# Kernel tuning notes

Hardware: AMD Instinct MI355X
Metric: run time of the kernel (lower is better)

## Reference

```python
import jax, jax.numpy as jnp
import numpy as np

EMBED_DIM = 512
NUM_HEADS = 8
NUM_RULES = 16
HEAD_DIM = EMBED_DIM // NUM_HEADS


def setup_inputs() -> dict:
    key = jax.random.key(0)
    ks = jax.random.split(key, 10)
    B, S, E, H, R, D = 4, 2048, EMBED_DIM, NUM_HEADS, NUM_RULES, HEAD_DIM
    lim_q = 1.0 / np.sqrt(E)
    lim_v = 1.0 / np.sqrt(E)
    return {
        "query": jax.random.normal(ks[0], (B, S, E), jnp.float32),
        "key": jax.random.normal(ks[1], (B, S, E), jnp.float32),
        "value": jax.random.normal(ks[2], (B, S, E), jnp.float32),
        "Wq": jax.random.uniform(ks[3], (E, E), jnp.float32, -lim_q, lim_q),
        "bq": jax.random.uniform(ks[4], (E,), jnp.float32, -lim_q, lim_q),
        "Wv": jax.random.uniform(ks[5], (E * R, E), jnp.float32, -lim_v, lim_v),
        "bv": jax.random.uniform(ks[6], (E * R,), jnp.float32, -lim_v, lim_v),
        "Wo": jax.random.uniform(ks[7], (E, E), jnp.float32, -lim_q, lim_q),
        "bo": jax.random.uniform(ks[8], (E,), jnp.float32, -lim_q, lim_q),
        "rules_keys": 0.02 * jax.random.normal(ks[9], (H, R, D), jnp.float32),
        "rules_widths": jnp.ones((H, R, D), jnp.float32),
    }


def reference(query, key, value, Wq, bq, Wv, bv, Wo, bo, rules_keys, rules_widths):
    B, S, E = query.shape
    H, R, D = NUM_HEADS, NUM_RULES, HEAD_DIM
    scale = D ** -0.5
    # preprocessing_query: Linear + scale, split heads -> (b, h, s, d)
    q = (query @ Wq.T + bq) * scale
    q = q.reshape(B, S, H, D).transpose(0, 2, 1, 3)
    # custom_distance (l1): |q - rule_key| broadcast over rules -> (b, h, s, r, d)
    diff = jnp.abs(q[:, :, :, None, :] - rules_keys[None, :, None, :, :])
    # get_z_values: z = mean_d( -0.5 * (diff / width)^2 ) -> (b, h, s, r)
    z = -0.5 * jnp.mean(jnp.square(diff / rules_widths[None, :, None, :, :]), axis=-1)
    # softmax over rules (last dim), dropout is identity (p=0)
    attn = jax.nn.softmax(z, axis=-1)  # (b, h, s, r)
    # preprocessing_value: Linear(E -> E*R) + scale, 'b s (h d r) -> b s h d r'
    v = (value @ Wv.T + bv) * scale
    v = v.reshape(B, S, H, D, R)
    # Fnn_output = attn * v summed over rules -> (b, s, h, d)
    out = jnp.einsum("bhsr,bshdr->bshd", attn, v)
    # torch: (b,s,h,d).transpose(1,2).contiguous().view(b, -1, h*d)
    out = out.transpose(0, 2, 1, 3).reshape(B, -1, H * D)
    return out @ Wo.T + bo
```

## Files before the change

### kernel.cpp

```cpp
#include <hip/hip_runtime.h>
#include <stdint.h>

#define TOKENS 8192
#define EDIM 512
#define HNUM 8
#define RNUM 16
#define DDIM 64
#define KDIM 512

typedef short v8s __attribute__((ext_vector_type(8)));
typedef float v4f __attribute__((ext_vector_type(4)));

__device__ inline float b2f(unsigned short u) {
    union { unsigned int i; float f; } c; c.i = ((unsigned int)u) << 16; return c.f;
}
__device__ inline unsigned short f2b(float f) {
    union { float f; unsigned int i; } c; c.f = f;
    unsigned int i = c.i + 0x7fffu + ((c.i >> 16) & 1u);
    return (unsigned short)(i >> 16);
}

#define GLD16(dst, src) \
    __builtin_amdgcn_global_load_lds((__attribute__((address_space(1))) void*)(src), \
                                     (__attribute__((address_space(3))) void*)(dst), 16, 0, 0)

__global__ __launch_bounds__(256)
void cvt5(const float* __restrict__ s0, const float* __restrict__ s1,
          const float* __restrict__ s2, const float* __restrict__ s3,
          const float* __restrict__ s4,
          unsigned short* __restrict__ d0, unsigned short* __restrict__ d1,
          unsigned short* __restrict__ d2, unsigned short* __restrict__ d3,
          unsigned short* __restrict__ d4,
          int n0, int n1, int n2, int n3, int n4)
{
    const float* s; unsigned short* d; int n;
    switch (blockIdx.y) {
        case 0: s = s0; d = d0; n = n0; break;
        case 1: s = s1; d = d1; n = n1; break;
        case 2: s = s2; d = d2; n = n2; break;
        case 3: s = s3; d = d3; n = n3; break;
        default: s = s4; d = d4; n = n4; break;
    }
    size_t base = (size_t)blockIdx.x * 2048 + (size_t)threadIdx.x * 8;
    if (base >= (size_t)n) return;
    const float4* sp = (const float4*)(s + base);
    float4 f0 = sp[0], f1 = sp[1];
    v8s o;
    o[0] = (short)f2b(f0.x); o[1] = (short)f2b(f0.y);
    o[2] = (short)f2b(f0.z); o[3] = (short)f2b(f0.w);
    o[4] = (short)f2b(f1.x); o[5] = (short)f2b(f1.y);
    o[6] = (short)f2b(f1.z); o[7] = (short)f2b(f1.w);
    *(v8s*)(d + base) = o;
}

template <int MODE>
__global__ __launch_bounds__(256, 4)
void gemm64(const unsigned short* __restrict__ A,
            const unsigned short* __restrict__ B,
            const float* __restrict__ bias,
            float* __restrict__ outF,
            unsigned short* __restrict__ outH)
{
    __shared__ unsigned short As[64 * 32];
    __shared__ unsigned short Bs[64 * 32];

    const int tid  = threadIdx.x;
    const int w    = tid >> 6;
    const int lane = tid & 63;
    const int quad = lane >> 4;
    const int l16  = lane & 15;
    const int wm   = w >> 1, wn = w & 1;
    const int m0   = blockIdx.x * 64;
    const int n0   = blockIdx.y * 64;

    v4f acc[2][2];
#pragma unroll
    for (int i = 0; i < 2; ++i)
#pragma unroll
        for (int j = 0; j < 2; ++j)
            acc[i][j] = (v4f){0.f, 0.f, 0.f, 0.f};

    for (int kt = 0; kt < KDIM / 32; ++kt) {
        int c = w * 64 + lane;
        const unsigned short* sa = A + (size_t)(m0 + (c >> 2)) * KDIM + kt * 32 + (c & 3) * 8;
        GLD16(&As[w * 512], sa);
        const unsigned short* sb = B + (size_t)(n0 + (c >> 2)) * KDIM + kt * 32 + (c & 3) * 8;
        GLD16(&Bs[w * 512], sb);
        __syncthreads();

        v8s af[2], bf[2];
#pragma unroll
        for (int mt = 0; mt < 2; ++mt)
            af[mt] = *(const v8s*)&As[(wm * 32 + mt * 16 + l16) * 32 + quad * 8];
#pragma unroll
        for (int nt = 0; nt < 2; ++nt)
            bf[nt] = *(const v8s*)&Bs[(wn * 32 + nt * 16 + l16) * 32 + quad * 8];
#pragma unroll
        for (int mt = 0; mt < 2; ++mt)
#pragma unroll
            for (int nt = 0; nt < 2; ++nt)
                acc[mt][nt] = __builtin_amdgcn_mfma_f32_16x16x32_bf16(af[mt], bf[nt], acc[mt][nt], 0, 0, 0);
        __syncthreads();
    }

#pragma unroll
    for (int mt = 0; mt < 2; ++mt)
#pragma unroll
        for (int nt = 0; nt < 2; ++nt) {
            int col = n0 + wn * 32 + nt * 16 + l16;
            float bb = bias[col];
#pragma unroll
            for (int rg = 0; rg < 4; ++rg) {
                int row = m0 + wm * 32 + mt * 16 + quad * 4 + rg;
                float v = acc[mt][nt][rg] + bb;
                if (MODE == 0) outH[(size_t)row * EDIM + col] = f2b(v * 0.125f);
                else           outF[(size_t)row * EDIM + col] = v;
            }
        }
}

__global__ __launch_bounds__(256, 2)
void gemm_v(const unsigned short* __restrict__ A,
            const unsigned short* __restrict__ B,
            const float* __restrict__ bias,
            unsigned short* __restrict__ outH,
            const float* __restrict__ attn)
{
    __shared__ unsigned short As[128 * 32];
    __shared__ unsigned short Bs[128 * 32];
    __shared__ unsigned short Os[128 * 8];

    const int tid  = threadIdx.x;
    const int w    = tid >> 6;
    const int lane = tid & 63;
    const int quad = lane >> 4;
    const int l16  = lane & 15;
    const int wm   = w >> 1, wn = w & 1;
    const int m0   = blockIdx.x * 128;
    const int n0   = blockIdx.y * 128;

    v4f acc[4][4];
#pragma unroll
    for (int i = 0; i < 4; ++i)
#pragma unroll
        for (int j = 0; j < 4; ++j)
            acc[i][j] = (v4f){0.f, 0.f, 0.f, 0.f};

    for (int kt = 0; kt < KDIM / 32; ++kt) {
#pragma unroll
        for (int p = 0; p < 2; ++p) {
            int cb = w * 128 + p * 64;
            int c  = cb + lane;
            const unsigned short* sa = A + (size_t)(m0 + (c >> 2)) * KDIM + kt * 32 + (c & 3) * 8;
            GLD16(&As[cb * 8], sa);
            const unsigned short* sb = B + (size_t)(n0 + (c >> 2)) * KDIM + kt * 32 + (c & 3) * 8;
            GLD16(&Bs[cb * 8], sb);
        }
        __syncthreads();

        v8s af[4], bf[4];
#pragma unroll
        for (int mt = 0; mt < 4; ++mt)
            af[mt] = *(const v8s*)&As[(wm * 64 + mt * 16 + l16) * 32 + quad * 8];
#pragma unroll
        for (int nt = 0; nt < 4; ++nt)
            bf[nt] = *(const v8s*)&Bs[(wn * 64 + nt * 16 + l16) * 32 + quad * 8];
#pragma unroll
        for (int mt = 0; mt < 4; ++mt)
#pragma unroll
            for (int nt = 0; nt < 4; ++nt)
                acc[mt][nt] = __builtin_amdgcn_mfma_f32_16x16x32_bf16(af[mt], bf[nt], acc[mt][nt], 0, 0, 0);
        __syncthreads();
    }

    const int h  = m0 >> 10;
    const int d0 = (m0 >> 4) & 63;
    float4 bias4[4];
#pragma unroll
    for (int mt = 0; mt < 4; ++mt)
        bias4[mt] = *(const float4*)&bias[m0 + wm * 64 + mt * 16 + quad * 4];
#pragma unroll
    for (int nt = 0; nt < 4; ++nt) {
        int token = n0 + wn * 64 + nt * 16 + l16;
        float4 av = *(const float4*)&attn[(size_t)token * (HNUM * RNUM) + h * RNUM + quad * 4];
#pragma unroll
        for (int mt = 0; mt < 4; ++mt) {
            v4f a = acc[mt][nt];
            float val = (a[0] + bias4[mt].x) * av.x
                      + (a[1] + bias4[mt].y) * av.y
                      + (a[2] + bias4[mt].z) * av.z
                      + (a[3] + bias4[mt].w) * av.w;
            val += __shfl_xor(val, 16);
            val += __shfl_xor(val, 32);
            if (quad == 0)
                Os[(wn * 64 + nt * 16 + l16) * 8 + (wm * 4 + mt)] = f2b(val * 0.125f);
        }
    }
    __syncthreads();
    if (tid < 128) {
        int sg = n0 + tid;
        int g  = (sg >> 11) * 2048 + h * 256 + ((sg & 2047) >> 3);
        int j  = (sg & 7) * 64 + d0;
        *(v8s*)&outH[(size_t)g * EDIM + j] = *(const v8s*)&Os[tid * 8];
    }
}

#define RST 72
__global__ __launch_bounds__(256)
void rules_softmax(const unsigned short* __restrict__ q,
                   const float* __restrict__ rk,
                   const float* __restrict__ rw,
                   float* __restrict__ attn)
{
    __shared__ float ql[16 * RST];
    __shared__ float rkl[16 * RST];
    __shared__ float iwl[16 * RST];
    const int h   = blockIdx.y;
    const int t0  = blockIdx.x * 16;
    const int tid = threadIdx.x;

#pragma unroll
    for (int i = 0; i < 4; ++i) {
        int jj = tid + i * 256;
        int r = jj >> 6, d = jj & 63;
        rkl[r * RST + d] = rk[h * (RNUM * DDIM) + jj];
        float wv = rw[h * (RNUM * DDIM) + jj];
        iwl[r * RST + d] = 1.0f / (wv * wv);
    }
    {
        int jj = tid * 4;
        int row = jj >> 6, d = jj & 63;
        const unsigned short* src = q + (size_t)(t0 + row) * EDIM + h * DDIM + d;
        unsigned short u0 = src[0], u1 = src[1], u2 = src[2], u3 = src[3];
        ql[row * RST + d + 0] = b2f(u0);
        ql[row * RST + d + 1] = b2f(u1);
        ql[row * RST + d + 2] = b2f(u2);
        ql[row * RST + d + 3] = b2f(u3);
    }
    __syncthreads();

    const int tl = tid >> 4;
    const int r  = tid & 15;
    const float* qrow = &ql[tl * RST];
    const float* krow = &rkl[r * RST];
    const float* wrow = &iwl[r * RST];
    float z = 0.f;
#pragma unroll
    for (int d4 = 0; d4 < 16; ++d4) {
        float4 qv = *(const float4*)&qrow[d4 * 4];
        float4 kv = *(const float4*)&krow[d4 * 4];
        float4 wv = *(const float4*)&wrow[d4 * 4];
        float a0 = qv.x - kv.x; z += a0 * a0 * wv.x;
        float a1 = qv.y - kv.y; z += a1 * a1 * wv.y;
        float a2 = qv.z - kv.z; z += a2 * a2 * wv.z;
        float a3 = qv.w - kv.w; z += a3 * a3 * wv.w;
    }
    z *= (-0.5f / 64.f);
    float mx = z;
#pragma unroll
    for (int s = 1; s < 16; s <<= 1) mx = fmaxf(mx, __shfl_xor(mx, s));
    float e = __expf(z - mx);
    float sum = e;
#pragma unroll
    for (int s = 1; s < 16; s <<= 1) sum += __shfl_xor(sum, s);
    attn[(size_t)(t0 + tl) * (HNUM * RNUM) + h * RNUM + r] = e / sum;
}

extern "C" void kernel_launch(void* const* d_in, const int* in_sizes, int n_in,
                              void* d_out, int out_size, void* d_ws, size_t ws_size,
                              hipStream_t stream) {
    const float* query = (const float*)d_in[0];
    const float* value = (const float*)d_in[2];
    const float* Wq = (const float*)d_in[3];
    const float* bq = (const float*)d_in[4];
    const float* Wv = (const float*)d_in[5];
    const float* bv = (const float*)d_in[6];
    const float* Wo = (const float*)d_in[7];
    const float* bo = (const float*)d_in[8];
    const float* rk = (const float*)d_in[9];
    const float* rw = (const float*)d_in[10];

    char* ws = (char*)d_ws;
    unsigned short* qbf  = (unsigned short*)(ws);
    unsigned short* vbf  = (unsigned short*)(ws + (size_t)( 8 << 20));
    unsigned short* Wqb  = (unsigned short*)(ws + (size_t)(16 << 20));
    unsigned short* Wvb  = (unsigned short*)(ws + (size_t)(17 << 20));
    unsigned short* Wob  = (unsigned short*)(ws + (size_t)(25 << 20));
    unsigned short* out1 = (unsigned short*)(ws + (size_t)(26 << 20));
    unsigned short* qf   = (unsigned short*)(ws + (size_t)(34 << 20));
    float* attn          = (float*)(ws + (size_t)(42 << 20));

    dim3 blk(256);
    cvt5<<<dim3(2048, 5), blk, 0, stream>>>(query, value, Wv, Wq, Wo,
                                            qbf, vbf, Wvb, Wqb, Wob,
                                            TOKENS * EDIM, TOKENS * EDIM, EDIM * RNUM * EDIM,
                                            EDIM * EDIM, EDIM * EDIM);
    gemm64<0><<<dim3(TOKENS / 64, EDIM / 64), blk, 0, stream>>>(qbf, Wqb, bq, nullptr, qf);
    rules_softmax<<<dim3(TOKENS / 16, HNUM), blk, 0, stream>>>(qf, rk, rw, attn);
    gemm_v<<<dim3((EDIM * RNUM) / 128, TOKENS / 128), blk, 0, stream>>>(Wvb, vbf, bv, out1, attn);
    gemm64<2><<<dim3(TOKENS / 64, EDIM / 64), blk, 0, stream>>>(out1, Wob, bo, (float*)d_out, nullptr);
}
```

Baseline: 232.8 us.

## Fuse Q projection with rules softmax and deepen V-GEMM K tile with swizzle

The Q projection is merged with the rules-distance softmax into one kernel. It reads fp32 query and Wq directly, converts them to bf16 in registers and keeps q in shared memory, which removes the conversion pass, the qf round-trip through global memory and a separate launch. The value GEMM now loads a 64-wide K tile per iteration with an XOR-swizzled LDS layout, halving barrier count and reducing bank conflicts. In exchange, the fused kernel's loads are no longer direct-to-LDS, stay synchronous and are not double-buffered, and the doubled LDS in gemm_v may cut occupancy.

```diff
diff --git a/kernel.cpp b/kernel.cpp
--- a/kernel.cpp
+++ b/kernel.cpp
@@ -25,21 +25,17 @@
                                      (__attribute__((address_space(3))) void*)(dst), 16, 0, 0)
 
 __global__ __launch_bounds__(256)
-void cvt5(const float* __restrict__ s0, const float* __restrict__ s1,
-          const float* __restrict__ s2, const float* __restrict__ s3,
-          const float* __restrict__ s4,
+void cvt3(const float* __restrict__ s0, const float* __restrict__ s1,
+          const float* __restrict__ s2,
           unsigned short* __restrict__ d0, unsigned short* __restrict__ d1,
-          unsigned short* __restrict__ d2, unsigned short* __restrict__ d3,
-          unsigned short* __restrict__ d4,
-          int n0, int n1, int n2, int n3, int n4)
+          unsigned short* __restrict__ d2,
+          int n0, int n1, int n2)
 {
     const float* s; unsigned short* d; int n;
     switch (blockIdx.y) {
         case 0: s = s0; d = d0; n = n0; break;
         case 1: s = s1; d = d1; n = n1; break;
-        case 2: s = s2; d = d2; n = n2; break;
-        case 3: s = s3; d = d3; n = n3; break;
-        default: s = s4; d = d4; n = n4; break;
+        default: s = s2; d = d2; n = n2; break;
     }
     size_t base = (size_t)blockIdx.x * 2048 + (size_t)threadIdx.x * 8;
     if (base >= (size_t)n) return;
@@ -53,16 +49,21 @@
     *(v8s*)(d + base) = o;
 }
 
-template <int MODE>
+#define QST 40
+#define QSF 68
 __global__ __launch_bounds__(256, 4)
-void gemm64(const unsigned short* __restrict__ A,
-            const unsigned short* __restrict__ B,
-            const float* __restrict__ bias,
-            float* __restrict__ outF,
-            unsigned short* __restrict__ outH)
+void qrules(const float* __restrict__ query,
+            const float* __restrict__ Wq,
+            const float* __restrict__ bq,
+            const float* __restrict__ rk,
+            const float* __restrict__ rw,
+            float* __restrict__ attn)
 {
-    __shared__ unsigned short As[64 * 32];
-    __shared__ unsigned short Bs[64 * 32];
+    __shared__ unsigned short As[64 * QST];
+    __shared__ unsigned short Bs[64 * QST];
+    __shared__ float qs[64 * QSF];
+    __shared__ float rkl[16 * QSF];
+    __shared__ float iwl[16 * QSF];
 
     const int tid  = threadIdx.x;
     const int w    = tid >> 6;
@@ -70,8 +71,20 @@
     const int quad = lane >> 4;
     const int l16  = lane & 15;
     const int wm   = w >> 1, wn = w & 1;
-    const int m0   = blockIdx.x * 64;
-    const int n0   = blockIdx.y * 64;
+    const int t0   = blockIdx.x * 64;
+    const int h    = blockIdx.y;
+    const int n0   = h * 64;
+
+    {
+        int r = tid >> 4, d = (tid & 15) * 4;
+        float4 kv = *(const float4*)&rk[h * (RNUM * DDIM) + r * DDIM + d];
+        float4 wv = *(const float4*)&rw[h * (RNUM * DDIM) + r * DDIM + d];
+        *(float4*)&rkl[r * QSF + d] = kv;
+        float4 iw;
+        iw.x = 1.0f / (wv.x * wv.x); iw.y = 1.0f / (wv.y * wv.y);
+        iw.z = 1.0f / (wv.z * wv.z); iw.w = 1.0f / (wv.w * wv.w);
+        *(float4*)&iwl[r * QSF + d] = iw;
+    }
 
     v4f acc[2][2];
 #pragma unroll
@@ -80,43 +93,88 @@
         for (int j = 0; j < 2; ++j)
             acc[i][j] = (v4f){0.f, 0.f, 0.f, 0.f};
 
+    const int srow = tid >> 2;
+    const int scc  = tid & 3;
     for (int kt = 0; kt < KDIM / 32; ++kt) {
-        int c = w * 64 + lane;
-        const unsigned short* sa = A + (size_t)(m0 + (c >> 2)) * KDIM + kt * 32 + (c & 3) * 8;
-        GLD16(&As[w * 512], sa);
-        const unsigned short* sb = B + (size_t)(n0 + (c >> 2)) * KDIM + kt * 32 + (c & 3) * 8;
-        GLD16(&Bs[w * 512], sb);
+        {
+            const float* sa = query + (size_t)(t0 + srow) * KDIM + kt * 32 + scc * 8;
+            float4 a0 = *(const float4*)sa, a1 = *(const float4*)(sa + 4);
+            v8s oa;
+            oa[0] = (short)f2b(a0.x); oa[1] = (short)f2b(a0.y);
+            oa[2] = (short)f2b(a0.z); oa[3] = (short)f2b(a0.w);
+            oa[4] = (short)f2b(a1.x); oa[5] = (short)f2b(a1.y);
+            oa[6] = (short)f2b(a1.z); oa[7] = (short)f2b(a1.w);
+            const float* sb = Wq + (size_t)(n0 + srow) * KDIM + kt * 32 + scc * 8;
+            float4 b0 = *(const float4*)sb, b1 = *(const float4*)(sb + 4);
+            v8s ob;
+            ob[0] = (short)f2b(b0.x); ob[1] = (short)f2b(b0.y);
+            ob[2] = (short)f2b(b0.z); ob[3] = (short)f2b(b0.w);
+            ob[4] = (short)f2b(b1.x); ob[5] = (short)f2b(b1.y);
+            ob[6] = (short)f2b(b1.z); ob[7] = (short)f2b(b1.w);
+            __syncthreads();
+            *(v8s*)&As[srow * QST + scc * 8] = oa;
+            *(v8s*)&Bs[srow * QST + scc * 8] = ob;
+        }
         __syncthreads();
 
         v8s af[2], bf[2];
 #pragma unroll
         for (int mt = 0; mt < 2; ++mt)
-            af[mt] = *(const v8s*)&As[(wm * 32 + mt * 16 + l16) * 32 + quad * 8];
+            af[mt] = *(const v8s*)&As[(wm * 32 + mt * 16 + l16) * QST + quad * 8];
 #pragma unroll
         for (int nt = 0; nt < 2; ++nt)
-            bf[nt] = *(const v8s*)&Bs[(wn * 32 + nt * 16 + l16) * 32 + quad * 8];
+            bf[nt] = *(const v8s*)&Bs[(wn * 32 + nt * 16 + l16) * QST + quad * 8];
 #pragma unroll
         for (int mt = 0; mt < 2; ++mt)
 #pragma unroll
             for (int nt = 0; nt < 2; ++nt)
                 acc[mt][nt] = __builtin_amdgcn_mfma_f32_16x16x32_bf16(af[mt], bf[nt], acc[mt][nt], 0, 0, 0);
-        __syncthreads();
-    }
+    }
+    __syncthreads();
 
 #pragma unroll
     for (int mt = 0; mt < 2; ++mt)
 #pragma unroll
         for (int nt = 0; nt < 2; ++nt) {
-            int col = n0 + wn * 32 + nt * 16 + l16;
-            float bb = bias[col];
+            int col = wn * 32 + nt * 16 + l16;
+            float bb = bq[n0 + col];
 #pragma unroll
             for (int rg = 0; rg < 4; ++rg) {
-                int row = m0 + wm * 32 + mt * 16 + quad * 4 + rg;
-                float v = acc[mt][nt][rg] + bb;
-                if (MODE == 0) outH[(size_t)row * EDIM + col] = f2b(v * 0.125f);
-                else           outF[(size_t)row * EDIM + col] = v;
+                int row = wm * 32 + mt * 16 + quad * 4 + rg;
+                qs[row * QSF + col] = (acc[mt][nt][rg] + bb) * 0.125f;
             }
         }
+    __syncthreads();
+
+    const int grp = tid >> 4;
+    const int r   = tid & 15;
+    const float* krow = &rkl[r * QSF];
+    const float* wrow = &iwl[r * QSF];
+#pragma unroll
+    for (int p = 0; p < 4; ++p) {
+        int tok = p * 16 + grp;
+        const float* qrow = &qs[tok * QSF];
+        float z = 0.f;
+#pragma unroll
+        for (int d4 = 0; d4 < 16; ++d4) {
+            float4 qv = *(const float4*)&qrow[d4 * 4];
+            float4 kv = *(const float4*)&krow[d4 * 4];
+            float4 wv = *(const float4*)&wrow[d4 * 4];
+            float a0 = qv.x - kv.x; z += a0 * a0 * wv.x;
+            float a1 = qv.y - kv.y; z += a1 * a1 * wv.y;
+            float a2 = qv.z - kv.z; z += a2 * a2 * wv.z;
+            float a3 = qv.w - kv.w; z += a3 * a3 * wv.w;
+        }
+        z *= (-0.5f / 64.f);
+        float mx = z;
+#pragma unroll
+        for (int s = 1; s < 16; s <<= 1) mx = fmaxf(mx, __shfl_xor(mx, s));
+        float e = __expf(z - mx);
+        float sum = e;
+#pragma unroll
+        for (int s = 1; s < 16; s <<= 1) sum += __shfl_xor(sum, s);
+        attn[(size_t)(t0 + tok) * (HNUM * RNUM) + h * RNUM + r] = e / sum;
+    }
 }
 
 __global__ __launch_bounds__(256, 2)
@@ -126,8 +184,8 @@
             unsigned short* __restrict__ outH,
             const float* __restrict__ attn)
 {
-    __shared__ unsigned short As[128 * 32];
-    __shared__ unsigned short Bs[128 * 32];
+    __shared__ unsigned short As[128 * 64];
+    __shared__ unsigned short Bs[128 * 64];
     __shared__ unsigned short Os[128 * 8];
 
     const int tid  = threadIdx.x;
@@ -146,30 +204,39 @@
         for (int j = 0; j < 4; ++j)
             acc[i][j] = (v4f){0.f, 0.f, 0.f, 0.f};
 
-    for (int kt = 0; kt < KDIM / 32; ++kt) {
-#pragma unroll
-        for (int p = 0; p < 2; ++p) {
-            int cb = w * 128 + p * 64;
-            int c  = cb + lane;
-            const unsigned short* sa = A + (size_t)(m0 + (c >> 2)) * KDIM + kt * 32 + (c & 3) * 8;
+    for (int kt = 0; kt < KDIM / 64; ++kt) {
+#pragma unroll
+        for (int p = 0; p < 4; ++p) {
+            int cb  = w * 256 + p * 64;
+            int c   = cb + lane;
+            int row = c >> 3;
+            int cc  = (c & 7) ^ (row & 7);
+            const unsigned short* sa = A + (size_t)(m0 + row) * KDIM + kt * 64 + cc * 8;
             GLD16(&As[cb * 8], sa);
-            const unsigned short* sb = B + (size_t)(n0 + (c >> 2)) * KDIM + kt * 32 + (c & 3) * 8;
+            const unsigned short* sb = B + (size_t)(n0 + row) * KDIM + kt * 64 + cc * 8;
             GLD16(&Bs[cb * 8], sb);
         }
         __syncthreads();
 
-        v8s af[4], bf[4];
-#pragma unroll
-        for (int mt = 0; mt < 4; ++mt)
-            af[mt] = *(const v8s*)&As[(wm * 64 + mt * 16 + l16) * 32 + quad * 8];
-#pragma unroll
-        for (int nt = 0; nt < 4; ++nt)
-            bf[nt] = *(const v8s*)&Bs[(wn * 64 + nt * 16 + l16) * 32 + quad * 8];
-#pragma unroll
-        for (int mt = 0; mt < 4; ++mt)
-#pragma unroll
-            for (int nt = 0; nt < 4; ++nt)
-                acc[mt][nt] = __builtin_amdgcn_mfma_f32_16x16x32_bf16(af[mt], bf[nt], acc[mt][nt], 0, 0, 0);
+#pragma unroll
+        for (int kk = 0; kk < 2; ++kk) {
+            v8s af[4], bf[4];
+#pragma unroll
+            for (int mt = 0; mt < 4; ++mt) {
+                int swz = (kk * 4 + quad) ^ (l16 & 7);
+                af[mt] = *(const v8s*)&As[(wm * 64 + mt * 16 + l16) * 64 + swz * 8];
+            }
+#pragma unroll
+            for (int nt = 0; nt < 4; ++nt) {
+                int swz = (kk * 4 + quad) ^ (l16 & 7);
+                bf[nt] = *(const v8s*)&Bs[(wn * 64 + nt * 16 + l16) * 64 + swz * 8];
+            }
+#pragma unroll
+            for (int mt = 0; mt < 4; ++mt)
+#pragma unroll
+                for (int nt = 0; nt < 4; ++nt)
+                    acc[mt][nt] = __builtin_amdgcn_mfma_f32_16x16x32_bf16(af[mt], bf[nt], acc[mt][nt], 0, 0, 0);
+        }
         __syncthreads();
     }
 
@@ -205,65 +272,66 @@
     }
 }
 
-#define RST 72
-__global__ __launch_bounds__(256)
-void rules_softmax(const unsigned short* __restrict__ q,
-                   const float* __restrict__ rk,
-                   const float* __restrict__ rw,
-                   float* __restrict__ attn)
+__global__ __launch_bounds__(256, 4)
+void gemm_o(const unsigned short* __restrict__ A,
+            const unsigned short* __restrict__ B,
+            const float* __restrict__ bias,
+            float* __restrict__ outF)
 {
-    __shared__ float ql[16 * RST];
-    __shared__ float rkl[16 * RST];
-    __shared__ float iwl[16 * RST];
-    const int h   = blockIdx.y;
-    const int t0  = blockIdx.x * 16;
-    const int tid = threadIdx.x;
-
-#pragma unroll
-    for (int i = 0; i < 4; ++i) {
-        int jj = tid + i * 256;
-        int r = jj >> 6, d = jj & 63;
-        rkl[r * RST + d] = rk[h * (RNUM * DDIM) + jj];
-        float wv = rw[h * (RNUM * DDIM) + jj];
-        iwl[r * RST + d] = 1.0f / (wv * wv);
-    }
-    {
-        int jj = tid * 4;
-        int row = jj >> 6, d = jj & 63;
-        const unsigned short* src = q + (size_t)(t0 + row) * EDIM + h * DDIM + d;
-        unsigned short u0 = src[0], u1 = src[1], u2 = src[2], u3 = src[3];
-        ql[row * RST + d + 0] = b2f(u0);
-        ql[row * RST + d + 1] = b2f(u1);
-        ql[row * RST + d + 2] = b2f(u2);
-        ql[row * RST + d + 3] = b2f(u3);
-    }
-    __syncthreads();
-
-    const int tl = tid >> 4;
-    const int r  = tid & 15;
-    const float* qrow = &ql[tl * RST];
-    const float* krow = &rkl[r * RST];
-    const float* wrow = &iwl[r * RST];
-    float z = 0.f;
-#pragma unroll
-    for (int d4 = 0; d4 < 16; ++d4) {
-        float4 qv = *(const float4*)&qrow[d4 * 4];
-        float4 kv = *(const float4*)&krow[d4 * 4];
-        float4 wv = *(const float4*)&wrow[d4 * 4];
-        float a0 = qv.x - kv.x; z += a0 * a0 * wv.x;
-        float a1 = qv.y - kv.y; z += a1 * a1 * wv.y;
-        float a2 = qv.z - kv.z; z += a2 * a2 * wv.z;
-        float a3 = qv.w - kv.w; z += a3 * a3 * wv.w;
-    }
-    z *= (-0.5f / 64.f);
-    float mx = z;
-#pragma unroll
-    for (int s = 1; s < 16; s <<= 1) mx = fmaxf(mx, __shfl_xor(mx, s));
-    float e = __expf(z - mx);
-    float sum = e;
-#pragma unroll
-    for (int s = 1; s < 16; s <<= 1) sum += __shfl_xor(sum, s);
-    attn[(size_t)(t0 + tl) * (HNUM * RNUM) + h * RNUM + r] = e / sum;
+    __shared__ unsigned short As[64 * 32];
+    __shared__ unsigned short Bs[64 * 32];
+
+    const int tid  = threadIdx.x;
+    const int w    = tid >> 6;
+    const int lane = tid & 63;
+    const int quad = lane >> 4;
+    const int l16  = lane & 15;
+    const int wm   = w >> 1, wn = w & 1;
+    const int m0   = blockIdx.x * 64;
+    const int n0   = blockIdx.y * 64;
+
+    v4f acc[2][2];
+#pragma unroll
+    for (int i = 0; i < 2; ++i)
+#pragma unroll
+        for (int j = 0; j < 2; ++j)
+            acc[i][j] = (v4f){0.f, 0.f, 0.f, 0.f};
+
+    for (int kt = 0; kt < KDIM / 32; ++kt) {
+        int c = w * 64 + lane;
+        const unsigned short* sa = A + (size_t)(m0 + (c >> 2)) * KDIM + kt * 32 + (c & 3) * 8;
+        GLD16(&As[w * 512], sa);
+        const unsigned short* sb = B + (size_t)(n0 + (c >> 2)) * KDIM + kt * 32 + (c & 3) * 8;
+        GLD16(&Bs[w * 512], sb);
+        __syncthreads();
+
+        v8s af[2], bf[2];
+#pragma unroll
+        for (int mt = 0; mt < 2; ++mt)
+            af[mt] = *(const v8s*)&As[(wm * 32 + mt * 16 + l16) * 32 + quad * 8];
+#pragma unroll
+        for (int nt = 0; nt < 2; ++nt)
+            bf[nt] = *(const v8s*)&Bs[(wn * 32 + nt * 16 + l16) * 32 + quad * 8];
+#pragma unroll
+        for (int mt = 0; mt < 2; ++mt)
+#pragma unroll
+            for (int nt = 0; nt < 2; ++nt)
+                acc[mt][nt] = __builtin_amdgcn_mfma_f32_16x16x32_bf16(af[mt], bf[nt], acc[mt][nt], 0, 0, 0);
+        __syncthreads();
+    }
+
+#pragma unroll
+    for (int mt = 0; mt < 2; ++mt)
+#pragma unroll
+        for (int nt = 0; nt < 2; ++nt) {
+            int col = n0 + wn * 32 + nt * 16 + l16;
+            float bb = bias[col];
+#pragma unroll
+            for (int rg = 0; rg < 4; ++rg) {
+                int row = m0 + wm * 32 + mt * 16 + quad * 4 + rg;
+                outF[(size_t)row * EDIM + col] = acc[mt][nt][rg] + bb;
+            }
+        }
 }
 
 extern "C" void kernel_launch(void* const* d_in, const int* in_sizes, int n_in,
@@ -281,22 +349,16 @@
     const float* rw = (const float*)d_in[10];
 
     char* ws = (char*)d_ws;
-    unsigned short* qbf  = (unsigned short*)(ws);
-    unsigned short* vbf  = (unsigned short*)(ws + (size_t)( 8 << 20));
-    unsigned short* Wqb  = (unsigned short*)(ws + (size_t)(16 << 20));
-    unsigned short* Wvb  = (unsigned short*)(ws + (size_t)(17 << 20));
-    unsigned short* Wob  = (unsigned short*)(ws + (size_t)(25 << 20));
-    unsigned short* out1 = (unsigned short*)(ws + (size_t)(26 << 20));
-    unsigned short* qf   = (unsigned short*)(ws + (size_t)(34 << 20));
-    float* attn          = (float*)(ws + (size_t)(42 << 20));
+    unsigned short* vbf  = (unsigned short*)(ws);
+    unsigned short* Wvb  = (unsigned short*)(ws + (size_t)( 8 << 20));
+    unsigned short* Wob  = (unsigned short*)(ws + (size_t)(16 << 20));
+    unsigned short* out1 = (unsigned short*)(ws + (size_t)(17 << 20));
+    float* attn          = (float*)(ws + (size_t)(25 << 20));
 
     dim3 blk(256);
-    cvt5<<<dim3(2048, 5), blk, 0, stream>>>(query, value, Wv, Wq, Wo,
-                                            qbf, vbf, Wvb, Wqb, Wob,
-                                            TOKENS * EDIM, TOKENS * EDIM, EDIM * RNUM * EDIM,
-                                            EDIM * EDIM, EDIM * EDIM);
-    gemm64<0><<<dim3(TOKENS / 64, EDIM / 64), blk, 0, stream>>>(qbf, Wqb, bq, nullptr, qf);
-    rules_softmax<<<dim3(TOKENS / 16, HNUM), blk, 0, stream>>>(qf, rk, rw, attn);
+    cvt3<<<dim3(2048, 3), blk, 0, stream>>>(value, Wv, Wo, vbf, Wvb, Wob,
+                                            TOKENS * EDIM, EDIM * RNUM * EDIM, EDIM * EDIM);
+    qrules<<<dim3(TOKENS / 64, HNUM), blk, 0, stream>>>(query, Wq, bq, rk, rw, attn);
     gemm_v<<<dim3((EDIM * RNUM) / 128, TOKENS / 128), blk, 0, stream>>>(Wvb, vbf, bv, out1, attn);
-    gemm64<2><<<dim3(TOKENS / 64, EDIM / 64), blk, 0, stream>>>(out1, Wob, bo, (float*)d_out, nullptr);
-}
+    gemm_o<<<dim3(TOKENS / 64, EDIM / 64), blk, 0, stream>>>(out1, Wob, bo, (float*)d_out);
+}
```

After: 364.0 us. +56.4%, slower.
